# Kernel tuning notes

Measured on AMD Instinct MI355X. Metric: run time of the kernel, lower is better.

The kernel has to match this reference:

```python
import jax, jax.numpy as jnp
import numpy as np

ATT_SIZE = 32
HEAD_NUM = 2


def setup_inputs() -> dict:
    key = jax.random.key(0)
    k_in, k_q, k_k, k_v, k_r = jax.random.split(key, 5)
    B, F, D = 16384, 32, 64
    H = ATT_SIZE * HEAD_NUM  # 64
    inputs = jax.random.normal(k_in, (B, F, D), dtype=jnp.float32)
    W_Query = jax.random.truncated_normal(k_q, -2.0, 2.0, (D, H), dtype=jnp.float32) * 0.05
    W_Key = jax.random.truncated_normal(k_k, -2.0, 2.0, (D, H), dtype=jnp.float32) * 0.05
    W_Value = jax.random.truncated_normal(k_v, -2.0, 2.0, (D, H), dtype=jnp.float32) * 0.05
    W_Res = jax.random.truncated_normal(k_r, -2.0, 2.0, (D, H), dtype=jnp.float32) * 0.05
    return {"inputs": inputs, "W_Query": W_Query, "W_Key": W_Key, "W_Value": W_Value, "W_Res": W_Res}


def reference(inputs, W_Query, W_Key, W_Value, W_Res):
    B, F, D = inputs.shape
    h, a = HEAD_NUM, ATT_SIZE
    # project and reshape to [B, h, F, a]
    q = jnp.einsum('bfd,de->bfe', inputs, W_Query).reshape(B, F, h, a).transpose(0, 2, 1, 3)
    k = jnp.einsum('bfd,de->bfe', inputs, W_Key).reshape(B, F, h, a).transpose(0, 2, 1, 3)
    v = jnp.einsum('bfd,de->bfe', inputs, W_Value).reshape(B, F, h, a).transpose(0, 2, 1, 3)
    # NOTE: original code has NO 1/sqrt(d) scaling
    scores = jnp.einsum('bhqa,bhka->bhqk', q, k)
    attn = jax.nn.softmax(scores, axis=-1)
    out = jnp.einsum('bhqk,bhka->bhqa', attn, v)  # [B, h, F, a]
    out = out.transpose(0, 2, 1, 3).reshape(B, F, h * a)
    out = out + jnp.einsum('bfd,de->bfe', inputs, W_Res)
    return jax.nn.relu(out)
```

## Files before the change

kernel.cpp:

```cpp
#include <hip/hip_runtime.h>


constexpr int kF = 32, kD = 64, kH = 64;

constexpr int XS = 72;
constexpr int QS = 72;
constexpr int VS = 40;
constexpr int PS = 40;

using short8  = __attribute__((ext_vector_type(8))) short;
using float4v = __attribute__((ext_vector_type(4))) float;

__device__ __forceinline__ unsigned short f2bf(float x) {
    unsigned u = __float_as_uint(x);
    u += 0x7FFF + ((u >> 16) & 1);
    return (unsigned short)(u >> 16);
}
__device__ __forceinline__ float bf2f(unsigned short b) {
    return __uint_as_float((unsigned)b << 16);
}

__global__ void wprep_kernel(const float* __restrict__ Wq, const float* __restrict__ Wk,
                             const float* __restrict__ Wv, const float* __restrict__ Wr,
                             unsigned short* __restrict__ wt) {
    const int m = blockIdx.x;
    const float* __restrict__ W = (m == 0) ? Wq : (m == 1) ? Wk : (m == 2) ? Wv : Wr;
    for (int i = threadIdx.x; i < kD * kH; i += blockDim.x) {
        const int e = i >> 6, d = i & 63;
        wt[m * kD * kH + e * kD + d] = f2bf(W[d * kH + e]);
    }
}

__global__ __launch_bounds__(256)
void interact_mfma(const float* __restrict__ X, const unsigned short* __restrict__ Wt,
                   float* __restrict__ out)
{
    __shared__ __align__(16) unsigned short s_x [kF * XS];
    __shared__ __align__(16) unsigned short s_q [kF * QS];
    __shared__ __align__(16) unsigned short s_k [kF * QS];
    __shared__ __align__(16) unsigned short s_r [kF * QS];
    __shared__ __align__(16) unsigned short s_vt[kH * VS];
    __shared__ __align__(16) unsigned short s_p [2 * kF * PS];

    const int t    = threadIdx.x;
    const int w    = t >> 6;
    const int lane = t & 63;
    const int quad = lane >> 4;
    const int l    = lane & 15;
    const int b    = blockIdx.x;

    short8 bfrag[4][2];
    {
        const unsigned short* __restrict__ wtm = Wt + w * (kD * kH);
        #pragma unroll
        for (int nt = 0; nt < 4; ++nt)
            #pragma unroll
            for (int ks = 0; ks < 2; ++ks)
                bfrag[nt][ks] =
                    *reinterpret_cast<const short8*>(wtm + (16 * nt + l) * kD + 32 * ks + quad * 8);
    }

    const float* __restrict__ Xb = X + (size_t)b * (kF * kD);
    #pragma unroll
    for (int i = 0; i < 2; ++i) {
        const int idx = i * 256 + t;
        const int f = idx >> 4, c = idx & 15;
        const float4 v = reinterpret_cast<const float4*>(Xb)[idx];
        ushort4 pk;
        pk.x = f2bf(v.x); pk.y = f2bf(v.y); pk.z = f2bf(v.z); pk.w = f2bf(v.w);
        *reinterpret_cast<ushort4*>(&s_x[f * XS + c * 4]) = pk;
    }
    __syncthreads();

    {
        float4v acc[2][4];
        #pragma unroll
        for (int mt = 0; mt < 2; ++mt)
            #pragma unroll
            for (int nt = 0; nt < 4; ++nt)
                acc[mt][nt] = (float4v){0.f, 0.f, 0.f, 0.f};

        short8 afrag[2][2];
        #pragma unroll
        for (int mt = 0; mt < 2; ++mt)
            #pragma unroll
            for (int ks = 0; ks < 2; ++ks)
                afrag[mt][ks] =
                    *reinterpret_cast<const short8*>(&s_x[(16 * mt + l) * XS + 32 * ks + quad * 8]);

        #pragma unroll
        for (int mt = 0; mt < 2; ++mt)
            #pragma unroll
            for (int nt = 0; nt < 4; ++nt) {
                acc[mt][nt] = __builtin_amdgcn_mfma_f32_16x16x32_bf16(
                    afrag[mt][0], bfrag[nt][0], acc[mt][nt], 0, 0, 0);
                acc[mt][nt] = __builtin_amdgcn_mfma_f32_16x16x32_bf16(
                    afrag[mt][1], bfrag[nt][1], acc[mt][nt], 0, 0, 0);
            }

        if (w == 2) {
            #pragma unroll
            for (int mt = 0; mt < 2; ++mt)
                #pragma unroll
                for (int nt = 0; nt < 4; ++nt)
                    #pragma unroll
                    for (int r = 0; r < 4; ++r)
                        s_vt[(16 * nt + l) * VS + 16 * mt + quad * 4 + r] = f2bf(acc[mt][nt][r]);
        } else {
            unsigned short* __restrict__ dst = (w == 0) ? s_q : (w == 1) ? s_k : s_r;
            #pragma unroll
            for (int mt = 0; mt < 2; ++mt)
                #pragma unroll
                for (int nt = 0; nt < 4; ++nt)
                    #pragma unroll
                    for (int r = 0; r < 4; ++r)
                        dst[(16 * mt + quad * 4 + r) * QS + 16 * nt + l] = f2bf(acc[mt][nt][r]);
        }
    }
    __syncthreads();

    const int h  = w >> 1;
    const int mt = w & 1;
    float inv[4];
    {
        const short8 qa =
            *reinterpret_cast<const short8*>(&s_q[(16 * mt + l) * QS + 32 * h + quad * 8]);
        const short8 kb0 =
            *reinterpret_cast<const short8*>(&s_k[(l) * QS + 32 * h + quad * 8]);
        const short8 kb1 =
            *reinterpret_cast<const short8*>(&s_k[(16 + l) * QS + 32 * h + quad * 8]);

        float4v s0 = (float4v){0.f, 0.f, 0.f, 0.f};
        float4v s1 = (float4v){0.f, 0.f, 0.f, 0.f};
        s0 = __builtin_amdgcn_mfma_f32_16x16x32_bf16(qa, kb0, s0, 0, 0, 0);
        s1 = __builtin_amdgcn_mfma_f32_16x16x32_bf16(qa, kb1, s1, 0, 0, 0);

        #pragma unroll
        for (int r = 0; r < 4; ++r) {
            float m = fmaxf(s0[r], s1[r]);
            #pragma unroll
            for (int d = 1; d < 16; d <<= 1) m = fmaxf(m, __shfl_xor(m, d));
            const float e0 = __expf(s0[r] - m);
            const float e1 = __expf(s1[r] - m);
            float sum = e0 + e1;
            #pragma unroll
            for (int d = 1; d < 16; d <<= 1) sum += __shfl_xor(sum, d);
            inv[r] = 1.0f / sum;
            const int row = 16 * mt + quad * 4 + r;
            s_p[(h * kF + row) * PS + l]      = f2bf(e0);
            s_p[(h * kF + row) * PS + 16 + l] = f2bf(e1);
        }
    }
    __syncthreads();

    {
        const short8 pa =
            *reinterpret_cast<const short8*>(&s_p[(h * kF + 16 * mt + l) * PS + quad * 8]);
        const short8 vb0 =
            *reinterpret_cast<const short8*>(&s_vt[(32 * h + l) * VS + quad * 8]);
        const short8 vb1 =
            *reinterpret_cast<const short8*>(&s_vt[(32 * h + 16 + l) * VS + quad * 8]);

        float4v o0 = (float4v){0.f, 0.f, 0.f, 0.f};
        float4v o1 = (float4v){0.f, 0.f, 0.f, 0.f};
        o0 = __builtin_amdgcn_mfma_f32_16x16x32_bf16(pa, vb0, o0, 0, 0, 0);
        o1 = __builtin_amdgcn_mfma_f32_16x16x32_bf16(pa, vb1, o1, 0, 0, 0);

        float* __restrict__ Ob = out + (size_t)b * (kF * kH);
        #pragma unroll
        for (int r = 0; r < 4; ++r) {
            const int f = 16 * mt + quad * 4 + r;
            const float rv0 = bf2f(s_r[f * QS + 32 * h + l]);
            const float rv1 = bf2f(s_r[f * QS + 32 * h + 16 + l]);
            Ob[f * kH + 32 * h + l]      = fmaxf(o0[r] * inv[r] + rv0, 0.0f);
            Ob[f * kH + 32 * h + 16 + l] = fmaxf(o1[r] * inv[r] + rv1, 0.0f);
        }
    }
}

extern "C" void kernel_launch(void* const* d_in, const int* in_sizes, int n_in,
                              void* d_out, int out_size, void* d_ws, size_t ws_size,
                              hipStream_t stream) {
    const float* X  = (const float*)d_in[0];
    const float* Wq = (const float*)d_in[1];
    const float* Wk = (const float*)d_in[2];
    const float* Wv = (const float*)d_in[3];
    const float* Wr = (const float*)d_in[4];
    float* out = (float*)d_out;
    unsigned short* wt = (unsigned short*)d_ws;

    wprep_kernel<<<4, 256, 0, stream>>>(Wq, Wk, Wv, Wr, wt);

    const int B = in_sizes[0] / (kF * kD);
    interact_mfma<<<B, 256, 0, stream>>>(X, wt, out);
}
```

Baseline: 279.5 us.

## Alias X/P LDS buffers, store V and residual transposed, drop a barrier

The bf16 X staging buffer is now reused for the softmax probabilities, and the residual projection is stored transposed with packed 4-wide writes, as V already was. This shrinks the per-block LDS footprint, which may let more blocks fit per CU, and cuts the number of scalar LDS stores. The barrier between writing P and reading it is removed, since each wave reads only the rows it wrote. Float-to-bf16 conversion now uses the native cast and the softmax reciprocal uses the hardware rcp, which is slightly less precise than a true division.

```diff
diff --git a/kernel.cpp b/kernel.cpp
--- a/kernel.cpp
+++ b/kernel.cpp
@@ -8,13 +8,12 @@
 constexpr int VS = 40;
 constexpr int PS = 40;
 
-using short8  = __attribute__((ext_vector_type(8))) short;
-using float4v = __attribute__((ext_vector_type(4))) float;
+using short8   = __attribute__((ext_vector_type(8))) short;
+using float4v  = __attribute__((ext_vector_type(4))) float;
+using ushort4v = __attribute__((ext_vector_type(4))) unsigned short;
 
 __device__ __forceinline__ unsigned short f2bf(float x) {
-    unsigned u = __float_as_uint(x);
-    u += 0x7FFF + ((u >> 16) & 1);
-    return (unsigned short)(u >> 16);
+    return __builtin_bit_cast(unsigned short, (__bf16)x);
 }
 __device__ __forceinline__ float bf2f(unsigned short b) {
     return __uint_as_float((unsigned)b << 16);
@@ -35,12 +34,11 @@
 void interact_mfma(const float* __restrict__ X, const unsigned short* __restrict__ Wt,
                    float* __restrict__ out)
 {
-    __shared__ __align__(16) unsigned short s_x [kF * XS];
+    __shared__ __align__(16) unsigned short s_xp[2 * kF * PS];
     __shared__ __align__(16) unsigned short s_q [kF * QS];
     __shared__ __align__(16) unsigned short s_k [kF * QS];
-    __shared__ __align__(16) unsigned short s_r [kF * QS];
     __shared__ __align__(16) unsigned short s_vt[kH * VS];
-    __shared__ __align__(16) unsigned short s_p [2 * kF * PS];
+    __shared__ __align__(16) unsigned short s_rt[kH * VS];
 
     const int t    = threadIdx.x;
     const int w    = t >> 6;
@@ -66,9 +64,8 @@
         const int idx = i * 256 + t;
         const int f = idx >> 4, c = idx & 15;
         const float4 v = reinterpret_cast<const float4*>(Xb)[idx];
-        ushort4 pk;
-        pk.x = f2bf(v.x); pk.y = f2bf(v.y); pk.z = f2bf(v.z); pk.w = f2bf(v.w);
-        *reinterpret_cast<ushort4*>(&s_x[f * XS + c * 4]) = pk;
+        ushort4v pk = { f2bf(v.x), f2bf(v.y), f2bf(v.z), f2bf(v.w) };
+        *reinterpret_cast<ushort4v*>(&s_xp[f * XS + c * 4]) = pk;
     }
     __syncthreads();
 
@@ -86,7 +83,7 @@
             #pragma unroll
             for (int ks = 0; ks < 2; ++ks)
                 afrag[mt][ks] =
-                    *reinterpret_cast<const short8*>(&s_x[(16 * mt + l) * XS + 32 * ks + quad * 8]);
+                    *reinterpret_cast<const short8*>(&s_xp[(16 * mt + l) * XS + 32 * ks + quad * 8]);
 
         #pragma unroll
         for (int mt = 0; mt < 2; ++mt)
@@ -98,16 +95,8 @@
                     afrag[mt][1], bfrag[nt][1], acc[mt][nt], 0, 0, 0);
             }
 
-        if (w == 2) {
-            #pragma unroll
-            for (int mt = 0; mt < 2; ++mt)
-                #pragma unroll
-                for (int nt = 0; nt < 4; ++nt)
-                    #pragma unroll
-                    for (int r = 0; r < 4; ++r)
-                        s_vt[(16 * nt + l) * VS + 16 * mt + quad * 4 + r] = f2bf(acc[mt][nt][r]);
-        } else {
-            unsigned short* __restrict__ dst = (w == 0) ? s_q : (w == 1) ? s_k : s_r;
+        if (w < 2) {
+            unsigned short* __restrict__ dst = (w == 0) ? s_q : s_k;
             #pragma unroll
             for (int mt = 0; mt < 2; ++mt)
                 #pragma unroll
@@ -115,6 +104,17 @@
                     #pragma unroll
                     for (int r = 0; r < 4; ++r)
                         dst[(16 * mt + quad * 4 + r) * QS + 16 * nt + l] = f2bf(acc[mt][nt][r]);
+        } else {
+            unsigned short* __restrict__ dstT = (w == 2) ? s_vt : s_rt;
+            #pragma unroll
+            for (int mt = 0; mt < 2; ++mt)
+                #pragma unroll
+                for (int nt = 0; nt < 4; ++nt) {
+                    ushort4v pk = { f2bf(acc[mt][nt][0]), f2bf(acc[mt][nt][1]),
+                                    f2bf(acc[mt][nt][2]), f2bf(acc[mt][nt][3]) };
+                    *reinterpret_cast<ushort4v*>(
+                        &dstT[(16 * nt + l) * VS + 16 * mt + 4 * quad]) = pk;
+                }
         }
     }
     __syncthreads();
@@ -145,17 +145,16 @@
             float sum = e0 + e1;
             #pragma unroll
             for (int d = 1; d < 16; d <<= 1) sum += __shfl_xor(sum, d);
-            inv[r] = 1.0f / sum;
+            inv[r] = __builtin_amdgcn_rcpf(sum);
             const int row = 16 * mt + quad * 4 + r;
-            s_p[(h * kF + row) * PS + l]      = f2bf(e0);
-            s_p[(h * kF + row) * PS + 16 + l] = f2bf(e1);
+            s_xp[(h * kF + row) * PS + l]      = f2bf(e0);
+            s_xp[(h * kF + row) * PS + 16 + l] = f2bf(e1);
         }
     }
-    __syncthreads();
 
     {
         const short8 pa =
-            *reinterpret_cast<const short8*>(&s_p[(h * kF + 16 * mt + l) * PS + quad * 8]);
+            *reinterpret_cast<const short8*>(&s_xp[(h * kF + 16 * mt + l) * PS + quad * 8]);
         const short8 vb0 =
             *reinterpret_cast<const short8*>(&s_vt[(32 * h + l) * VS + quad * 8]);
         const short8 vb1 =
@@ -166,14 +165,17 @@
         o0 = __builtin_amdgcn_mfma_f32_16x16x32_bf16(pa, vb0, o0, 0, 0, 0);
         o1 = __builtin_amdgcn_mfma_f32_16x16x32_bf16(pa, vb1, o1, 0, 0, 0);
 
+        const ushort4v rA =
+            *reinterpret_cast<const ushort4v*>(&s_rt[(32 * h + l) * VS + 16 * mt + 4 * quad]);
+        const ushort4v rB =
+            *reinterpret_cast<const ushort4v*>(&s_rt[(32 * h + 16 + l) * VS + 16 * mt + 4 * quad]);
+
         float* __restrict__ Ob = out + (size_t)b * (kF * kH);
         #pragma unroll
         for (int r = 0; r < 4; ++r) {
             const int f = 16 * mt + quad * 4 + r;
-            const float rv0 = bf2f(s_r[f * QS + 32 * h + l]);
-            const float rv1 = bf2f(s_r[f * QS + 32 * h + 16 + l]);
-            Ob[f * kH + 32 * h + l]      = fmaxf(o0[r] * inv[r] + rv0, 0.0f);
-            Ob[f * kH + 32 * h + 16 + l] = fmaxf(o1[r] * inv[r] + rv1, 0.0f);
+            Ob[f * kH + 32 * h + l]      = fmaxf(o0[r] * inv[r] + bf2f(rA[r]), 0.0f);
+            Ob[f * kH + 32 * h + 16 + l] = fmaxf(o1[r] * inv[r] + bf2f(rB[r]), 0.0f);
         }
     }
 }
```

Measured after the change: 271.3 us. 2.9% less time.
